# Kernel optimization log

Hardware: AMD Instinct MI355X
Metric: run time of the kernel (lower is better)

The kernel has to match this reference:

```python
import jax, jax.numpy as jnp
import numpy as np

N_NODES = 500_000
N_EDGES = 5_000_000
D = 16


def setup_inputs() -> dict:
    key = jax.random.key(0)
    k1, k2, k3, k4 = jax.random.split(key, 4)
    x = jax.random.normal(k1, (N_NODES, D), dtype=jnp.float32)
    edge_index = jax.random.randint(k2, (2, N_EDGES), 0, N_NODES, dtype=jnp.int32)
    # SAGEConv params: lin_l (applied to aggregated neighbors, carries bias),
    # lin_r (applied to root/self features, no bias). Torch Linear stores W as [out, in].
    scale = 1.0 / np.sqrt(D)
    W_l = jax.random.uniform(k3, (D, D), minval=-scale, maxval=scale, dtype=jnp.float32)
    b_l = jnp.zeros((D,), dtype=jnp.float32)
    W_r = jax.random.uniform(k4, (D, D), minval=-scale, maxval=scale, dtype=jnp.float32)
    return {"x": x, "edge_index": edge_index, "W_l": W_l, "b_l": b_l, "W_r": W_r}


def reference(x, edge_index, W_l, b_l, W_r):
    src = edge_index[0]  # message sources (x_j)
    dst = edge_index[1]  # aggregation targets (i)
    n = x.shape[0]
    # mean aggregation of neighbor features per destination node
    agg = jax.ops.segment_sum(x[src], dst, num_segments=n)  # [N, D]
    cnt = jax.ops.segment_sum(jnp.ones((src.shape[0],), dtype=x.dtype), dst, num_segments=n)
    mean = agg / jnp.maximum(cnt, 1.0)[:, None]
    # out = lin_l(mean) + lin_r(x)
    return mean @ W_l.T + b_l + x @ W_r.T
```

## Files before the change

kernel.cpp:

```cpp
#include <hip/hip_runtime.h>

#define N_NODES 500000
#define N_EDGES 5000000
#define D 16

__global__ void sage_scatter(const float* __restrict__ x,
                             const int* __restrict__ esrc,
                             const int* __restrict__ edst,
                             float* __restrict__ agg,
                             float* __restrict__ cnt) {
    long long gid = (long long)blockIdx.x * blockDim.x + threadIdx.x;
    long long e = gid >> 4;
    int d = (int)(gid & 15);
    if (e >= N_EDGES) return;
    int s = esrc[e];
    int t = edst[e];
    atomicAdd(&agg[(long long)t * D + d], x[(long long)s * D + d]);
    if (d == 0) atomicAdd(&cnt[t], 1.0f);
}

__global__ void sage_finalize(const float* __restrict__ x,
                              float* __restrict__ agg_out,
                              const float* __restrict__ cnt,
                              const float* __restrict__ W_l,
                              const float* __restrict__ b_l,
                              const float* __restrict__ W_r) {
    __shared__ float sWl[D * D];
    __shared__ float sWr[D * D];
    __shared__ float sb[D];
    int tid = threadIdx.x;
    if (tid < D * D) {
        sWl[tid] = W_l[tid];
        sWr[tid] = W_r[tid];
    }
    if (tid < D) sb[tid] = b_l[tid];
    __syncthreads();

    int i = blockIdx.x * blockDim.x + tid;
    if (i >= N_NODES) return;

    float inv = 1.0f / fmaxf(cnt[i], 1.0f);

    float m[D], xv[D];
    const float4* ap = (const float4*)(agg_out + (long long)i * D);
    const float4* xp = (const float4*)(x + (long long)i * D);
#pragma unroll
    for (int q = 0; q < 4; ++q) {
        float4 a = ap[q];
        float4 b = xp[q];
        m[4 * q + 0] = a.x * inv; m[4 * q + 1] = a.y * inv;
        m[4 * q + 2] = a.z * inv; m[4 * q + 3] = a.w * inv;
        xv[4 * q + 0] = b.x; xv[4 * q + 1] = b.y;
        xv[4 * q + 2] = b.z; xv[4 * q + 3] = b.w;
    }

    float o[D];
#pragma unroll
    for (int oo = 0; oo < D; ++oo) {
        float acc = sb[oo];
#pragma unroll
        for (int k = 0; k < D; ++k)
            acc += m[k] * sWl[oo * D + k] + xv[k] * sWr[oo * D + k];
        o[oo] = acc;
    }

    float4* op = (float4*)(agg_out + (long long)i * D);
#pragma unroll
    for (int q = 0; q < 4; ++q)
        op[q] = make_float4(o[4 * q + 0], o[4 * q + 1], o[4 * q + 2], o[4 * q + 3]);
}

extern "C" void kernel_launch(void* const* d_in, const int* in_sizes, int n_in,
                              void* d_out, int out_size, void* d_ws, size_t ws_size,
                              hipStream_t stream) {
    const float* x   = (const float*)d_in[0];
    const int*   ei  = (const int*)d_in[1];
    const float* W_l = (const float*)d_in[2];
    const float* b_l = (const float*)d_in[3];
    const float* W_r = (const float*)d_in[4];

    float* agg_out = (float*)d_out;
    float* cnt     = (float*)d_ws;

    hipMemsetAsync(agg_out, 0, (size_t)N_NODES * D * sizeof(float), stream);
    hipMemsetAsync(cnt, 0, (size_t)N_NODES * sizeof(float), stream);

    const int block = 256;
    long long total = (long long)N_EDGES * D;
    unsigned grid1 = (unsigned)((total + block - 1) / block);
    sage_scatter<<<grid1, block, 0, stream>>>(x, ei, ei + N_EDGES, agg_out, cnt);

    unsigned grid2 = (N_NODES + block - 1) / block;
    sage_finalize<<<grid2, block, 0, stream>>>(x, agg_out, cnt, W_l, b_l, W_r);
}
```

Baseline: 535.4 us.

## Replace float atomic scatter with CSR build and per-node gather

Builds a CSR-style edge list grouped by destination: it counts in-degrees with int atomics, turns them into offsets with a block scan, then fills source slots. A fused kernel then has 16 lanes per node gather neighbor features, take the mean and apply both linear layers, so the 80M float atomics on the output go away. In exchange it adds several kernel launches, two passes of int atomics over the edges, and a scan. Per-node gather cost varies with degree, and the slot order within a node depends on atomic timing, which can change the float summation order. The old scatter path is kept as a fallback when the workspace is too small.

```diff
diff --git a/kernel.cpp b/kernel.cpp
--- a/kernel.cpp
+++ b/kernel.cpp
@@ -3,72 +3,163 @@
 #define N_NODES 500000
 #define N_EDGES 5000000
 #define D 16
-
-__global__ void sage_scatter(const float* __restrict__ x,
-                             const int* __restrict__ esrc,
-                             const int* __restrict__ edst,
-                             float* __restrict__ agg,
+#define SCAN_B 512
+#define NBLK ((N_NODES + SCAN_B - 1) / SCAN_B)
+
+
+__global__ void count_k(const int* __restrict__ edst, int* __restrict__ cnt) {
+    int e = blockIdx.x * blockDim.x + threadIdx.x;
+    if (e < N_EDGES) atomicAdd(&cnt[edst[e]], 1);
+}
+
+__global__ void block_sums_k(const int* __restrict__ cnt, int* __restrict__ bsum) {
+    __shared__ int ws[8];
+    int t = threadIdx.x;
+    int i = blockIdx.x * SCAN_B + t;
+    int v = (i < N_NODES) ? cnt[i] : 0;
+#pragma unroll
+    for (int off = 32; off; off >>= 1) v += __shfl_down(v, off, 64);
+    if ((t & 63) == 0) ws[t >> 6] = v;
+    __syncthreads();
+    if (t == 0) {
+        int s = 0;
+#pragma unroll
+        for (int j = 0; j < 8; ++j) s += ws[j];
+        bsum[blockIdx.x] = s;
+    }
+}
+
+__global__ void scan_bsums_k(int* __restrict__ bsum) {
+    __shared__ int s[1024];
+    int t = threadIdx.x;
+    int v = (t < NBLK) ? bsum[t] : 0;
+    s[t] = v;
+    __syncthreads();
+    for (int off = 1; off < 1024; off <<= 1) {
+        int u = (t >= off) ? s[t - off] : 0;
+        __syncthreads();
+        s[t] += u;
+        __syncthreads();
+    }
+    if (t < NBLK) bsum[t] = s[t] - v;
+}
+
+__global__ void scan_offsets_k(const int* __restrict__ cnt, const int* __restrict__ bsum,
+                               int* __restrict__ offs) {
+    __shared__ int s[SCAN_B];
+    int b = blockIdx.x, t = threadIdx.x;
+    int i = b * SCAN_B + t;
+    int v = (i < N_NODES) ? cnt[i] : 0;
+    s[t] = v;
+    __syncthreads();
+    for (int off = 1; off < SCAN_B; off <<= 1) {
+        int u = (t >= off) ? s[t - off] : 0;
+        __syncthreads();
+        s[t] += u;
+        __syncthreads();
+    }
+    if (i < N_NODES) offs[i] = bsum[b] + (s[t] - v);
+}
+
+__global__ void fill_slots_k(const int* __restrict__ esrc, const int* __restrict__ edst,
+                             const int* __restrict__ offs, int* __restrict__ cursor,
+                             int* __restrict__ slots) {
+    int e = blockIdx.x * blockDim.x + threadIdx.x;
+    if (e >= N_EDGES) return;
+    int t = edst[e];
+    int p = atomicAdd(&cursor[t], 1);
+    slots[offs[t] + p] = esrc[e];
+}
+
+__global__ __launch_bounds__(256) void gather_finalize_k(
+    const float* __restrict__ x, const int* __restrict__ slots,
+    const int* __restrict__ offs, const int* __restrict__ cnt,
+    const float* __restrict__ W_l, const float* __restrict__ b_l,
+    const float* __restrict__ W_r, float* __restrict__ out) {
+    int tid = blockIdx.x * blockDim.x + threadIdx.x;
+    int g = tid >> 4;
+    int d = tid & 15;
+    if (g >= N_NODES) return;
+
+    float wl[D], wr[D];
+    const float4* wl4 = (const float4*)(W_l + d * D);
+    const float4* wr4 = (const float4*)(W_r + d * D);
+#pragma unroll
+    for (int q = 0; q < 4; ++q) {
+        float4 a = wl4[q], b = wr4[q];
+        wl[4*q+0]=a.x; wl[4*q+1]=a.y; wl[4*q+2]=a.z; wl[4*q+3]=a.w;
+        wr[4*q+0]=b.x; wr[4*q+1]=b.y; wr[4*q+2]=b.z; wr[4*q+3]=b.w;
+    }
+
+    int beg = offs[g], n = cnt[g];
+    float acc = 0.f;
+    for (int e0 = 0; e0 < n; e0 += 16) {
+        int c = n - e0; if (c > 16) c = 16;
+        int myslot = (d < c) ? slots[beg + e0 + d] : 0;
+        for (int e = 0; e < c; ++e) {
+            int s = __shfl(myslot, e, 16);
+            acc += x[s * D + d];
+        }
+    }
+    float m  = acc / fmaxf((float)n, 1.0f);
+    float xv = x[g * D + d];
+
+    float o = b_l[d];
+#pragma unroll
+    for (int k = 0; k < D; ++k) {
+        float mk = __shfl(m, k, 16);
+        float xk = __shfl(xv, k, 16);
+        o += mk * wl[k] + xk * wr[k];
+    }
+    out[g * D + d] = o;
+}
+
+
+__global__ void sage_scatter(const float* __restrict__ x, const int* __restrict__ esrc,
+                             const int* __restrict__ edst, float* __restrict__ agg,
                              float* __restrict__ cnt) {
     long long gid = (long long)blockIdx.x * blockDim.x + threadIdx.x;
     long long e = gid >> 4;
     int d = (int)(gid & 15);
     if (e >= N_EDGES) return;
-    int s = esrc[e];
-    int t = edst[e];
-    atomicAdd(&agg[(long long)t * D + d], x[(long long)s * D + d]);
-    if (d == 0) atomicAdd(&cnt[t], 1.0f);
-}
-
-__global__ void sage_finalize(const float* __restrict__ x,
-                              float* __restrict__ agg_out,
-                              const float* __restrict__ cnt,
-                              const float* __restrict__ W_l,
-                              const float* __restrict__ b_l,
-                              const float* __restrict__ W_r) {
-    __shared__ float sWl[D * D];
-    __shared__ float sWr[D * D];
-    __shared__ float sb[D];
+    atomicAdd(&agg[(long long)edst[e] * D + d], x[(long long)esrc[e] * D + d]);
+    if (d == 0) atomicAdd(&cnt[edst[e]], 1.0f);
+}
+
+__global__ void sage_finalize(const float* __restrict__ x, float* __restrict__ agg_out,
+                              const float* __restrict__ cnt, const float* __restrict__ W_l,
+                              const float* __restrict__ b_l, const float* __restrict__ W_r) {
+    __shared__ float sWl[D * D], sWr[D * D], sb[D];
     int tid = threadIdx.x;
-    if (tid < D * D) {
-        sWl[tid] = W_l[tid];
-        sWr[tid] = W_r[tid];
-    }
+    if (tid < D * D) { sWl[tid] = W_l[tid]; sWr[tid] = W_r[tid]; }
     if (tid < D) sb[tid] = b_l[tid];
     __syncthreads();
-
     int i = blockIdx.x * blockDim.x + tid;
     if (i >= N_NODES) return;
-
     float inv = 1.0f / fmaxf(cnt[i], 1.0f);
-
     float m[D], xv[D];
     const float4* ap = (const float4*)(agg_out + (long long)i * D);
     const float4* xp = (const float4*)(x + (long long)i * D);
 #pragma unroll
     for (int q = 0; q < 4; ++q) {
-        float4 a = ap[q];
-        float4 b = xp[q];
-        m[4 * q + 0] = a.x * inv; m[4 * q + 1] = a.y * inv;
-        m[4 * q + 2] = a.z * inv; m[4 * q + 3] = a.w * inv;
-        xv[4 * q + 0] = b.x; xv[4 * q + 1] = b.y;
-        xv[4 * q + 2] = b.z; xv[4 * q + 3] = b.w;
-    }
-
+        float4 a = ap[q], b = xp[q];
+        m[4*q+0]=a.x*inv; m[4*q+1]=a.y*inv; m[4*q+2]=a.z*inv; m[4*q+3]=a.w*inv;
+        xv[4*q+0]=b.x; xv[4*q+1]=b.y; xv[4*q+2]=b.z; xv[4*q+3]=b.w;
+    }
     float o[D];
 #pragma unroll
     for (int oo = 0; oo < D; ++oo) {
-        float acc = sb[oo];
-#pragma unroll
-        for (int k = 0; k < D; ++k)
-            acc += m[k] * sWl[oo * D + k] + xv[k] * sWr[oo * D + k];
-        o[oo] = acc;
-    }
-
+        float a2 = sb[oo];
+#pragma unroll
+        for (int k = 0; k < D; ++k) a2 += m[k]*sWl[oo*D+k] + xv[k]*sWr[oo*D+k];
+        o[oo] = a2;
+    }
     float4* op = (float4*)(agg_out + (long long)i * D);
 #pragma unroll
     for (int q = 0; q < 4; ++q)
-        op[q] = make_float4(o[4 * q + 0], o[4 * q + 1], o[4 * q + 2], o[4 * q + 3]);
-}
+        op[q] = make_float4(o[4*q+0], o[4*q+1], o[4*q+2], o[4*q+3]);
+}
+
 
 extern "C" void kernel_launch(void* const* d_in, const int* in_sizes, int n_in,
                               void* d_out, int out_size, void* d_ws, size_t ws_size,
@@ -78,18 +169,36 @@
     const float* W_l = (const float*)d_in[2];
     const float* b_l = (const float*)d_in[3];
     const float* W_r = (const float*)d_in[4];
-
-    float* agg_out = (float*)d_out;
-    float* cnt     = (float*)d_ws;
-
-    hipMemsetAsync(agg_out, 0, (size_t)N_NODES * D * sizeof(float), stream);
-    hipMemsetAsync(cnt, 0, (size_t)N_NODES * sizeof(float), stream);
-
-    const int block = 256;
-    long long total = (long long)N_EDGES * D;
-    unsigned grid1 = (unsigned)((total + block - 1) / block);
-    sage_scatter<<<grid1, block, 0, stream>>>(x, ei, ei + N_EDGES, agg_out, cnt);
-
-    unsigned grid2 = (N_NODES + block - 1) / block;
-    sage_finalize<<<grid2, block, 0, stream>>>(x, agg_out, cnt, W_l, b_l, W_r);
-}
+    const int* esrc = ei;
+    const int* edst = ei + N_EDGES;
+    float* out = (float*)d_out;
+
+    size_t need = ((size_t)3 * N_NODES + 1024 + N_EDGES) * sizeof(int);
+
+    if (ws_size >= need) {
+        int* cnt    = (int*)d_ws;
+        int* offs   = cnt + N_NODES;
+        int* cursor = offs + N_NODES;
+        int* bsum   = cursor + N_NODES;
+        int* slots  = bsum + 1024;
+
+        hipMemsetAsync(cnt, 0, (size_t)N_NODES * sizeof(int), stream);
+        hipMemsetAsync(cursor, 0, (size_t)N_NODES * sizeof(int), stream);
+
+        count_k<<<(N_EDGES + 255) / 256, 256, 0, stream>>>(edst, cnt);
+        block_sums_k<<<NBLK, SCAN_B, 0, stream>>>(cnt, bsum);
+        scan_bsums_k<<<1, 1024, 0, stream>>>(bsum);
+        scan_offsets_k<<<NBLK, SCAN_B, 0, stream>>>(cnt, bsum, offs);
+        fill_slots_k<<<(N_EDGES + 255) / 256, 256, 0, stream>>>(esrc, edst, offs, cursor, slots);
+
+        unsigned grid = (unsigned)(((long long)N_NODES * D + 255) / 256);
+        gather_finalize_k<<<grid, 256, 0, stream>>>(x, slots, offs, cnt, W_l, b_l, W_r, out);
+    } else {
+        float* cntf = (float*)d_ws;
+        hipMemsetAsync(out, 0, (size_t)N_NODES * D * sizeof(float), stream);
+        hipMemsetAsync(cntf, 0, (size_t)N_NODES * sizeof(float), stream);
+        long long total = (long long)N_EDGES * D;
+        sage_scatter<<<(unsigned)((total + 255) / 256), 256, 0, stream>>>(x, esrc, edst, out, cntf);
+        sage_finalize<<<(N_NODES + 255) / 256, 256, 0, stream>>>(x, out, cntf, W_l, b_l, W_r);
+    }
+}
```

Result: slower. 610.2 us (+14.0%).

## Bin edges by destination block and reduce in shared memory with fp16 gathers

Applied to the files above, without the earlier changes.

Replaces global float atomics with a bucket sort: histogram edges by 128-node destination blocks, scan, and scatter packed (local dst, src) records. Each block then accumulates its bucket into a shared-memory slice with LDS atomics and applies the two linear layers in place, fusing the finalize step. Source features are gathered from an fp16 copy of x when workspace allows, which halves gather bandwidth but loses precision in the aggregation. The new path needs roughly 20MB+ of workspace and adds several small kernels, including a single-block scan.

```diff
diff --git a/kernel.cpp b/kernel.cpp
--- a/kernel.cpp
+++ b/kernel.cpp
@@ -1,73 +1,159 @@
 #include <hip/hip_runtime.h>
+#include <hip/hip_fp16.h>
 
 #define N_NODES 500000
 #define N_EDGES 5000000
 #define D 16
-
-__global__ void sage_scatter(const float* __restrict__ x,
-                             const int* __restrict__ esrc,
-                             const int* __restrict__ edst,
-                             float* __restrict__ agg,
+#define BSHIFT 7
+#define BSIZE 128
+#define NB ((N_NODES + BSIZE - 1) / BSIZE)
+#define CPAD 16
+
+__global__ void tohalf_k(const float* __restrict__ x, __half2* __restrict__ xh) {
+    int i = blockIdx.x * blockDim.x + threadIdx.x;
+    if (i >= (N_NODES * D) / 4) return;
+    float4 v = ((const float4*)x)[i];
+    xh[2 * i]     = __floats2half2_rn(v.x, v.y);
+    xh[2 * i + 1] = __floats2half2_rn(v.z, v.w);
+}
+
+__global__ __launch_bounds__(256) void hist_k(const int* __restrict__ edst,
+                                              int* __restrict__ bhist) {
+    __shared__ int h[NB];
+    for (int i = threadIdx.x; i < NB; i += 256) h[i] = 0;
+    __syncthreads();
+    int stride = gridDim.x * blockDim.x;
+    for (int e = blockIdx.x * blockDim.x + threadIdx.x; e < N_EDGES; e += stride)
+        atomicAdd(&h[edst[e] >> BSHIFT], 1);
+    __syncthreads();
+    for (int i = threadIdx.x; i < NB; i += 256)
+        if (h[i]) atomicAdd(&bhist[i * CPAD], h[i]);
+}
+
+__global__ void scan_k(const int* __restrict__ bhist, int* __restrict__ boff,
+                       int* __restrict__ bcur) {
+    __shared__ int s[1024];
+    int t = threadIdx.x;
+    int v[4]; int sum = 0;
+#pragma unroll
+    for (int j = 0; j < 4; ++j) { int i = 4 * t + j; v[j] = (i < NB) ? bhist[i * CPAD] : 0; sum += v[j]; }
+    s[t] = sum; __syncthreads();
+    for (int off = 1; off < 1024; off <<= 1) {
+        int u = (t >= off) ? s[t - off] : 0;
+        __syncthreads(); s[t] += u; __syncthreads();
+    }
+    int base = s[t] - sum;
+#pragma unroll
+    for (int j = 0; j < 4; ++j) {
+        int i = 4 * t + j;
+        if (i < NB) { boff[i] = base; bcur[i * CPAD] = base; }
+        base += v[j];
+    }
+    if (t == 1023) boff[NB] = s[1023];
+}
+
+__global__ void binscatter_k(const int* __restrict__ esrc, const int* __restrict__ edst,
+                             int* __restrict__ bcur, unsigned* __restrict__ rec) {
+    int e = blockIdx.x * blockDim.x + threadIdx.x;
+    if (e >= N_EDGES) return;
+    int t = edst[e];
+    int p = atomicAdd(&bcur[(t >> BSHIFT) * CPAD], 1);
+    rec[p] = ((unsigned)(t & (BSIZE - 1)) << 19) | (unsigned)esrc[e];
+}
+
+template <int USE_H>
+__global__ __launch_bounds__(256) void reduce_k(
+    const float* __restrict__ x, const __half* __restrict__ xh,
+    const unsigned* __restrict__ rec, const int* __restrict__ boff,
+    const float* __restrict__ Wl, const float* __restrict__ bl,
+    const float* __restrict__ Wr, float* __restrict__ out) {
+    __shared__ float slice[BSIZE * D];
+    __shared__ int scnt[BSIZE];
+    int tid = threadIdx.x;
+    for (int i = tid; i < BSIZE * D; i += 256) slice[i] = 0.f;
+    if (tid < BSIZE) scnt[tid] = 0;
+    __syncthreads();
+
+    int d = tid & 15, g = tid >> 4;
+    float wl[D], wr[D];
+    const float4* wl4 = (const float4*)(Wl + d * D);
+    const float4* wr4 = (const float4*)(Wr + d * D);
+#pragma unroll
+    for (int q = 0; q < 4; ++q) {
+        float4 a = wl4[q], b2 = wr4[q];
+        wl[4*q]=a.x; wl[4*q+1]=a.y; wl[4*q+2]=a.z; wl[4*q+3]=a.w;
+        wr[4*q]=b2.x; wr[4*q+1]=b2.y; wr[4*q+2]=b2.z; wr[4*q+3]=b2.w;
+    }
+
+    int b = blockIdx.x;
+    int beg = boff[b], end = boff[b + 1];
+    for (int r = beg + g; r < end; r += 16) {
+        unsigned rc = rec[r];
+        int src = (int)(rc & 0x7FFFFu);
+        int nl  = (int)(rc >> 19);
+        float v = USE_H ? __half2float(xh[src * D + d]) : x[src * D + d];
+        atomicAdd(&slice[nl * D + d], v);
+        if (d == 0) atomicAdd(&scnt[nl], 1);
+    }
+    __syncthreads();
+
+    int node0 = b << BSHIFT;
+    for (int n = g; n < BSIZE; n += 16) {
+        int node = node0 + n;
+        if (node >= N_NODES) continue;
+        float m  = slice[n * D + d] / fmaxf((float)scnt[n], 1.f);
+        float xv = x[node * D + d];
+        float o  = bl[d];
+#pragma unroll
+        for (int k = 0; k < D; ++k)
+            o += __shfl(m, k, 16) * wl[k] + __shfl(xv, k, 16) * wr[k];
+        out[node * D + d] = o;
+    }
+}
+
+__global__ void sage_scatter(const float* __restrict__ x, const int* __restrict__ esrc,
+                             const int* __restrict__ edst, float* __restrict__ agg,
                              float* __restrict__ cnt) {
     long long gid = (long long)blockIdx.x * blockDim.x + threadIdx.x;
     long long e = gid >> 4;
     int d = (int)(gid & 15);
     if (e >= N_EDGES) return;
-    int s = esrc[e];
-    int t = edst[e];
-    atomicAdd(&agg[(long long)t * D + d], x[(long long)s * D + d]);
-    if (d == 0) atomicAdd(&cnt[t], 1.0f);
-}
-
-__global__ void sage_finalize(const float* __restrict__ x,
-                              float* __restrict__ agg_out,
-                              const float* __restrict__ cnt,
-                              const float* __restrict__ W_l,
-                              const float* __restrict__ b_l,
-                              const float* __restrict__ W_r) {
-    __shared__ float sWl[D * D];
-    __shared__ float sWr[D * D];
-    __shared__ float sb[D];
+    atomicAdd(&agg[(long long)edst[e] * D + d], x[(long long)esrc[e] * D + d]);
+    if (d == 0) atomicAdd(&cnt[edst[e]], 1.0f);
+}
+
+__global__ void sage_finalize(const float* __restrict__ x, float* __restrict__ agg_out,
+                              const float* __restrict__ cnt, const float* __restrict__ W_l,
+                              const float* __restrict__ b_l, const float* __restrict__ W_r) {
+    __shared__ float sWl[D * D], sWr[D * D], sb[D];
     int tid = threadIdx.x;
-    if (tid < D * D) {
-        sWl[tid] = W_l[tid];
-        sWr[tid] = W_r[tid];
-    }
+    if (tid < D * D) { sWl[tid] = W_l[tid]; sWr[tid] = W_r[tid]; }
     if (tid < D) sb[tid] = b_l[tid];
     __syncthreads();
-
     int i = blockIdx.x * blockDim.x + tid;
     if (i >= N_NODES) return;
-
     float inv = 1.0f / fmaxf(cnt[i], 1.0f);
-
     float m[D], xv[D];
     const float4* ap = (const float4*)(agg_out + (long long)i * D);
     const float4* xp = (const float4*)(x + (long long)i * D);
 #pragma unroll
     for (int q = 0; q < 4; ++q) {
-        float4 a = ap[q];
-        float4 b = xp[q];
-        m[4 * q + 0] = a.x * inv; m[4 * q + 1] = a.y * inv;
-        m[4 * q + 2] = a.z * inv; m[4 * q + 3] = a.w * inv;
-        xv[4 * q + 0] = b.x; xv[4 * q + 1] = b.y;
-        xv[4 * q + 2] = b.z; xv[4 * q + 3] = b.w;
-    }
-
+        float4 a = ap[q], b = xp[q];
+        m[4*q]=a.x*inv; m[4*q+1]=a.y*inv; m[4*q+2]=a.z*inv; m[4*q+3]=a.w*inv;
+        xv[4*q]=b.x; xv[4*q+1]=b.y; xv[4*q+2]=b.z; xv[4*q+3]=b.w;
+    }
     float o[D];
 #pragma unroll
     for (int oo = 0; oo < D; ++oo) {
-        float acc = sb[oo];
-#pragma unroll
-        for (int k = 0; k < D; ++k)
-            acc += m[k] * sWl[oo * D + k] + xv[k] * sWr[oo * D + k];
-        o[oo] = acc;
-    }
-
+        float a2 = sb[oo];
+#pragma unroll
+        for (int k = 0; k < D; ++k) a2 += m[k]*sWl[oo*D+k] + xv[k]*sWr[oo*D+k];
+        o[oo] = a2;
+    }
     float4* op = (float4*)(agg_out + (long long)i * D);
 #pragma unroll
     for (int q = 0; q < 4; ++q)
-        op[q] = make_float4(o[4 * q + 0], o[4 * q + 1], o[4 * q + 2], o[4 * q + 3]);
+        op[q] = make_float4(o[4*q], o[4*q+1], o[4*q+2], o[4*q+3]);
 }
 
 extern "C" void kernel_launch(void* const* d_in, const int* in_sizes, int n_in,
@@ -78,18 +164,40 @@
     const float* W_l = (const float*)d_in[2];
     const float* b_l = (const float*)d_in[3];
     const float* W_r = (const float*)d_in[4];
-
-    float* agg_out = (float*)d_out;
-    float* cnt     = (float*)d_ws;
-
-    hipMemsetAsync(agg_out, 0, (size_t)N_NODES * D * sizeof(float), stream);
-    hipMemsetAsync(cnt, 0, (size_t)N_NODES * sizeof(float), stream);
-
-    const int block = 256;
-    long long total = (long long)N_EDGES * D;
-    unsigned grid1 = (unsigned)((total + block - 1) / block);
-    sage_scatter<<<grid1, block, 0, stream>>>(x, ei, ei + N_EDGES, agg_out, cnt);
-
-    unsigned grid2 = (N_NODES + block - 1) / block;
-    sage_finalize<<<grid2, block, 0, stream>>>(x, agg_out, cnt, W_l, b_l, W_r);
-}
+    const int* esrc = ei;
+    const int* edst = ei + N_EDGES;
+    float* out = (float*)d_out;
+
+    size_t rec_b  = (size_t)N_EDGES * 4;
+    size_t pad_b  = (size_t)NB * CPAD * 4;
+    size_t boff_b = (size_t)(NB + 1) * 4;
+    size_t base_need = rec_b + 2 * pad_b + boff_b;
+    size_t h_need    = base_need + (size_t)N_NODES * D * 2;
+
+    if (ws_size >= base_need) {
+        unsigned* rec  = (unsigned*)d_ws;
+        int* bhist = (int*)((char*)d_ws + rec_b);
+        int* bcur  = bhist + (size_t)NB * CPAD;
+        int* boff  = bcur + (size_t)NB * CPAD;
+        __half* xh = (__half*)((char*)d_ws + base_need);
+        int use_h = (ws_size >= h_need);
+
+        hipMemsetAsync(bhist, 0, pad_b, stream);
+        if (use_h)
+            tohalf_k<<<(N_NODES * D / 4 + 255) / 256, 256, 0, stream>>>(x, (__half2*)xh);
+        hist_k<<<512, 256, 0, stream>>>(edst, bhist);
+        scan_k<<<1, 1024, 0, stream>>>(bhist, boff, bcur);
+        binscatter_k<<<(N_EDGES + 255) / 256, 256, 0, stream>>>(esrc, edst, bcur, rec);
+        if (use_h)
+            reduce_k<1><<<NB, 256, 0, stream>>>(x, xh, rec, boff, W_l, b_l, W_r, out);
+        else
+            reduce_k<0><<<NB, 256, 0, stream>>>(x, xh, rec, boff, W_l, b_l, W_r, out);
+    } else {
+        float* cntf = (float*)d_ws;
+        hipMemsetAsync(out, 0, (size_t)N_NODES * D * sizeof(float), stream);
+        hipMemsetAsync(cntf, 0, (size_t)N_NODES * sizeof(float), stream);
+        long long total = (long long)N_EDGES * D;
+        sage_scatter<<<(unsigned)((total + 255) / 256), 256, 0, stream>>>(x, esrc, edst, out, cntf);
+        sage_finalize<<<(N_NODES + 255) / 256, 256, 0, stream>>>(x, out, cntf, W_l, b_l, W_r);
+    }
+}
```

New measurement: 939.6 us. +75.5%, slower.
